# Optimization experiments

Hardware: AMD Instinct MI355X
Metric: run time of the kernel (lower is better)

## Reference

```python
import jax, jax.numpy as jnp
import numpy as np

N_SLOTS = 64
DECAY = 0.999
B, S, H, M = 4, 4096, 2048, 128


def _l2norm(t, eps=1e-12):
    return t / jnp.maximum(jnp.linalg.norm(t, axis=-1, keepdims=True), eps)


def setup_inputs() -> dict:
    key = jax.random.key(0)
    ks = jax.random.split(key, 6)
    return {
        "x": jax.random.normal(ks[0], (B, S, H), dtype=jnp.float32),
        "W_query": jax.random.normal(ks[1], (M, H), dtype=jnp.float32) * 0.02,
        "W_key": jax.random.normal(ks[2], (M, H), dtype=jnp.float32) * 0.02,
        "W_value": jax.random.normal(ks[3], (M, H), dtype=jnp.float32) * 0.02,
        "W_out": jax.random.normal(ks[4], (H, M), dtype=jnp.float32) * 0.02,
        "W_gate_w": jax.random.normal(ks[5], (1, H), dtype=jnp.float32) * 0.02,
        "W_gate_b": jnp.full((1,), -2.0, dtype=jnp.float32),
        "log_beta": jnp.full((1,), np.log(8.0), dtype=jnp.float32),
        "chunk_size": 64,
    }


def reference(x, W_query, W_key, W_value, W_out, W_gate_w, W_gate_b, log_beta, chunk_size):
    b, s, h = x.shape
    m = W_query.shape[0]
    dt = x.dtype

    q = x @ W_query.T                      # (b, s, m)
    k = _l2norm(x @ W_key.T)               # (b, s, m)
    v = _l2norm(x @ W_value.T)             # (b, s, m)
    gate = jax.nn.sigmoid(x @ W_gate_w.T + W_gate_b)  # (b, s, 1)
    beta = jnp.exp(log_beta).reshape(())

    nc = s // chunk_size
    decay_c = jnp.asarray(DECAY, dt) ** chunk_size

    def chunkify(t):
        # (b, s, d) -> (nc, b, chunk, d)
        return jnp.moveaxis(t.reshape(b, nc, chunk_size, -1), 1, 0)

    qc, kc, vc = chunkify(q), chunkify(k), chunkify(v)
    wc = chunkify(gate)[..., 0]            # (nc, b, chunk)

    K0 = jnp.zeros((N_SLOTS, m), dt)
    V0 = jnp.zeros((N_SLOTS, m), dt)
    s0 = jnp.zeros((N_SLOTS,), dt)
    ptr0 = jnp.asarray(0, jnp.int32)

    def step(carry, inp):
        K_mem, V_mem, mem_strength, ptr = carry
        qch, kch, vch, wch = inp           # (b,c,m) x3, (b,c)
        # --- read: softmax retrieval over active slots ---
        slot_mask = (mem_strength > 1e-8).astype(dt)           # (n_slots,)
        scores = jnp.einsum("bcm,nm->bcn", qch, K_mem) * beta
        scores = scores + (1.0 - slot_mask) * -1e9
        attn = jax.nn.softmax(scores, axis=-1)
        r = jnp.einsum("bcn,nm->bcm", attn, V_mem)
        r = jnp.where(mem_strength.sum() < 1e-8, jnp.zeros_like(r), r)
        # --- write: gated aggregation into one slot ---
        w_sum = jnp.maximum(wch.sum(), 1e-8)
        k_agg = _l2norm((kch * wch[..., None]).sum((0, 1)) / w_sum)
        v_agg = _l2norm((vch * wch[..., None]).sum((0, 1)) / w_sum)
        write_str = wch.mean()
        mem_strength = mem_strength * decay_c
        slot = ptr % N_SLOTS
        K_mem = K_mem.at[slot].set(k_agg)
        V_mem = V_mem.at[slot].set(v_agg)
        mem_strength = mem_strength.at[slot].set(write_str)
        return (K_mem, V_mem, mem_strength, ptr + 1), (r, write_str)

    _, (rs, wss) = jax.lax.scan(step, (K0, V0, s0, ptr0), (qc, kc, vc, wc))

    retrieved = jnp.moveaxis(rs, 0, 1).reshape(b, s, m)
    out = retrieved @ W_out.T              # (b, s, h)
    # clamp output norm to 10
    onorm = jnp.maximum(jnp.linalg.norm(out, axis=-1, keepdims=True), 1e-6)
    out = out * jnp.minimum(10.0 / onorm, 1.0)
    mean_ws = jnp.mean(wss)
    return out, mean_ws
```

## Files before the change

### kernel.cpp

```cpp
#include <hip/hip_runtime.h>
#include <math.h>
#include <stdint.h>

#define NTOK 16384
#define SEQ  4096
#define HD   2048
#define MD   128
#define NCH  64
#define CHK  64

typedef __attribute__((ext_vector_type(8))) _Float16 half8;
typedef __attribute__((ext_vector_type(4))) float floatx4;

__device__ __forceinline__ void gload_lds16(const void* g, void* l) {
    __builtin_amdgcn_global_load_lds(
        (const __attribute__((address_space(1))) unsigned int*)(uintptr_t)g,
        (__attribute__((address_space(3))) unsigned int*)(uintptr_t)l,
        16, 0, 0);
}

__global__ __launch_bounds__(256) void convert_w_kernel(
    const float* __restrict__ Wq, const float* __restrict__ Wk,
    const float* __restrict__ Wv, const float* __restrict__ Wo,
    _Float16* __restrict__ Wcath, _Float16* __restrict__ Woh)
{
    int i = blockIdx.x * 256 + threadIdx.x;
    if (i < 384 * HD) {
        int r = i >> 11;
        float val;
        if (r < 128)      val = Wq[i];
        else if (r < 256) val = Wk[i - 128 * HD];
        else              val = Wv[i - 256 * HD];
        Wcath[i] = (_Float16)val;
    } else {
        int j = i - 384 * HD;
        Woh[j] = (_Float16)Wo[j];
    }
}

__global__ __launch_bounds__(128) void gmat_kernel(
    const float* __restrict__ Wo, float* __restrict__ G)
{
    __shared__ float col[HD];
    int a = blockIdx.x;
    int b = threadIdx.x;
    for (int j = b; j < HD; j += 128) col[j] = Wo[(size_t)j * MD + a];
    __syncthreads();
    float s = 0.f;
    for (int j = 0; j < HD; ++j) s = fmaf(col[j], Wo[(size_t)j * MD + b], s);
    G[a * MD + b] = s;
}

__global__ __launch_bounds__(256) void gemm_proj_mfma(
    const float* __restrict__ x, const _Float16* __restrict__ Wcath,
    const float* __restrict__ Wgw, const float* __restrict__ gb,
    float* __restrict__ q, float* __restrict__ k, float* __restrict__ v,
    float* __restrict__ wg)
{
    __shared__ _Float16 As[2048], Bs[4096];
    floatx4 acc[2][4];
    #pragma unroll
    for (int i = 0; i < 2; ++i)
        #pragma unroll
        for (int j = 0; j < 4; ++j) acc[i][j] = (floatx4){0.f, 0.f, 0.f, 0.f};

    const int tid  = threadIdx.x;
    const int wave = tid >> 6, lane = tid & 63;
    const int wm = wave & 1, wn = wave >> 1;
    const int seg_r = lane >> 2;
    const int chunk = lane & 3;
    const int arow  = tid >> 2;
    const int acol  = tid & 3;
    const int row0 = blockIdx.x * 64;
    const int col0 = blockIdx.y * 128;
    const bool do_gate = (blockIdx.y == 0);

    float gacc = 0.f;

    for (int k0 = 0; k0 < HD; k0 += 32) {
        #pragma unroll
        for (int rnd = 0; rnd < 2; ++rnd) {
            int s = wave + 4 * rnd;
            int r = s * 16 + seg_r;
            gload_lds16(Wcath + (size_t)(col0 + r) * HD + k0 + chunk * 8,
                        Bs + s * 512);
        }
        const float* ap = x + (size_t)(row0 + arow) * HD + k0 + acol * 8;
        float4 a0 = *(const float4*)(ap);
        float4 a1 = *(const float4*)(ap + 4);
        if (do_gate) {
            const float* wp = Wgw + k0 + acol * 8;
            float4 w0 = *(const float4*)(wp);
            float4 w1 = *(const float4*)(wp + 4);
            gacc += a0.x * w0.x + a0.y * w0.y + a0.z * w0.z + a0.w * w0.w
                  + a1.x * w1.x + a1.y * w1.y + a1.z * w1.z + a1.w * w1.w;
        }
        half8 h0;
        h0[0] = (_Float16)a0.x; h0[1] = (_Float16)a0.y;
        h0[2] = (_Float16)a0.z; h0[3] = (_Float16)a0.w;
        h0[4] = (_Float16)a1.x; h0[5] = (_Float16)a1.y;
        h0[6] = (_Float16)a1.z; h0[7] = (_Float16)a1.w;
        *(half8*)&As[arow * 32 + acol * 8] = h0;

        __syncthreads();
        half8 af[2], bf[4];
        #pragma unroll
        for (int i = 0; i < 2; ++i)
            af[i] = *(const half8*)&As[(wm * 32 + i * 16 + (lane & 15)) * 32 + (lane >> 4) * 8];
        #pragma unroll
        for (int j = 0; j < 4; ++j)
            bf[j] = *(const half8*)&Bs[(wn * 64 + j * 16 + (lane & 15)) * 32 + (lane >> 4) * 8];
        #pragma unroll
        for (int i = 0; i < 2; ++i)
            #pragma unroll
            for (int j = 0; j < 4; ++j)
                acc[i][j] = __builtin_amdgcn_mfma_f32_16x16x32_f16(
                    af[i], bf[j], acc[i][j], 0, 0, 0);
        __syncthreads();
    }

    if (do_gate) {
        float g4 = gacc + __shfl_xor(gacc, 1);
        g4 += __shfl_xor(g4, 2);
        if (acol == 0) {
            int row = row0 + arow;
            wg[row] = 1.f / (1.f + expf(-(g4 + gb[0])));
        }
    }

    float* dst = (blockIdx.y == 0) ? q : ((blockIdx.y == 1) ? k : v);
    #pragma unroll
    for (int i = 0; i < 2; ++i) {
        int m = row0 + wm * 32 + i * 16 + (lane >> 4) * 4;
        #pragma unroll
        for (int j = 0; j < 4; ++j) {
            int c = wn * 64 + j * 16 + (lane & 15);
            #pragma unroll
            for (int r = 0; r < 4; ++r)
                dst[(size_t)(m + r) * MD + c] = acc[i][j][r];
        }
    }
}

__global__ __launch_bounds__(256) void normsig_kernel(
    float* __restrict__ k, float* __restrict__ v)
{
    int wave = threadIdx.x >> 6, lane = threadIdx.x & 63;
    int row = blockIdx.x * 4 + wave;
    size_t base = (size_t)row * MD + lane * 2;
    float2 k2 = *reinterpret_cast<float2*>(&k[base]);
    float2 v2 = *reinterpret_cast<float2*>(&v[base]);
    float ks = k2.x * k2.x + k2.y * k2.y;
    float vs = v2.x * v2.x + v2.y * v2.y;
    #pragma unroll
    for (int off = 32; off > 0; off >>= 1) {
        ks += __shfl_xor(ks, off);
        vs += __shfl_xor(vs, off);
    }
    float ki = 1.f / fmaxf(sqrtf(ks), 1e-12f);
    float vi = 1.f / fmaxf(sqrtf(vs), 1e-12f);
    k2.x *= ki; k2.y *= ki; v2.x *= vi; v2.y *= vi;
    *reinterpret_cast<float2*>(&k[base]) = k2;
    *reinterpret_cast<float2*>(&v[base]) = v2;
}

__global__ __launch_bounds__(256) void agg_part_kernel(
    const float* __restrict__ kn, const float* __restrict__ vn,
    const float* __restrict__ w,
    float* __restrict__ kpart, float* __restrict__ vpart,
    float* __restrict__ wpart)
{
    int t = blockIdx.x >> 2, b = blockIdx.x & 3;
    int tid = threadIdx.x;
    int d = tid & 127, h = tid >> 7;
    int base_row = b * SEQ + t * CHK;

    float ka = 0.f, va = 0.f;
    for (int c = h * 32; c < h * 32 + 32; ++c) {
        int row = base_row + c;
        float wv = w[row];
        ka = fmaf(wv, kn[(size_t)row * MD + d], ka);
        va = fmaf(wv, vn[(size_t)row * MD + d], va);
    }
    __shared__ float sk[128], sv[128];
    if (h == 1) { sk[d] = ka; sv[d] = va; }
    __syncthreads();
    if (h == 0) {
        kpart[(size_t)blockIdx.x * 128 + d] = ka + sk[d];
        vpart[(size_t)blockIdx.x * 128 + d] = va + sv[d];
    }
    if (tid < 64) {
        float wv = w[base_row + tid];
        #pragma unroll
        for (int off = 32; off > 0; off >>= 1) wv += __shfl_xor(wv, off);
        if (tid == 0) wpart[blockIdx.x] = wv;
    }
}

__global__ __launch_bounds__(128) void agg_combine_kernel(
    const float* __restrict__ kpart, const float* __restrict__ vpart,
    const float* __restrict__ wpart,
    float* __restrict__ kaT, float* __restrict__ vagg, float* __restrict__ wstr)
{
    int t = blockIdx.x;
    int d = threadIdx.x;
    int wave = d >> 6, lane = d & 63;
    float ku = 0.f, vu = 0.f;
    #pragma unroll
    for (int b = 0; b < 4; ++b) {
        ku += kpart[(size_t)(t * 4 + b) * 128 + d];
        vu += vpart[(size_t)(t * 4 + b) * 128 + d];
    }
    float wsum = wpart[t * 4] + wpart[t * 4 + 1] + wpart[t * 4 + 2] + wpart[t * 4 + 3];
    float winv = 1.f / fmaxf(wsum, 1e-8f);
    ku *= winv; vu *= winv;

    __shared__ float red[4];
    float ks = ku * ku, vs = vu * vu;
    #pragma unroll
    for (int off = 32; off > 0; off >>= 1) {
        ks += __shfl_xor(ks, off);
        vs += __shfl_xor(vs, off);
    }
    if (lane == 0) { red[wave] = ks; red[2 + wave] = vs; }
    __syncthreads();
    float kinv = 1.f / fmaxf(sqrtf(red[0] + red[1]), 1e-12f);
    float vinv = 1.f / fmaxf(sqrtf(red[2] + red[3]), 1e-12f);
    kaT[d * NCH + t] = ku * kinv;
    vagg[t * MD + d] = vu * vinv;
    if (d == 0) wstr[t] = wsum * (1.f / 256.f);
}

__global__ __launch_bounds__(64) void meanws_kernel(
    const float* __restrict__ wstr, float* __restrict__ outp)
{
    int lane = threadIdx.x;
    float v = wstr[lane];
    #pragma unroll
    for (int off = 32; off > 0; off >>= 1) v += __shfl_xor(v, off);
    if (lane == 0) outp[0] = v * (1.f / 64.f);
}

__global__ __launch_bounds__(256) void attn_kernel(
    const float* __restrict__ q, const float* __restrict__ kaT,
    const float* __restrict__ vagg, const float* __restrict__ G,
    const float* __restrict__ logbeta, _Float16* __restrict__ rsh16)
{
    __shared__ float qs[4][128];
    __shared__ float attn_s[4][64];
    __shared__ float rsh[4][128];
    int wave = threadIdx.x >> 6, lane = threadIdx.x & 63;
    int row = blockIdx.x * 4 + wave;
    int t = (row & (SEQ - 1)) >> 6;
    float beta = expf(logbeta[0]);

    qs[wave][lane]      = q[(size_t)row * MD + lane];
    qs[wave][lane + 64] = q[(size_t)row * MD + 64 + lane];
    __syncthreads();

    float sc = -INFINITY;
    if (lane < t) {
        sc = 0.f;
        for (int d = 0; d < 128; ++d)
            sc = fmaf(qs[wave][d], kaT[d * NCH + lane], sc);
        sc *= beta;
    }
    float mx = sc;
    #pragma unroll
    for (int off = 32; off > 0; off >>= 1) mx = fmaxf(mx, __shfl_xor(mx, off));
    float e = (lane < t) ? expf(sc - mx) : 0.f;
    float ssum = e;
    #pragma unroll
    for (int off = 32; off > 0; off >>= 1) ssum += __shfl_xor(ssum, off);
    float attn = (t > 0) ? (e / ssum) : 0.f;
    attn_s[wave][lane] = attn;
    __syncthreads();

    float r0 = 0.f, r1 = 0.f;
    for (int n = 0; n < t; ++n) {
        float a = attn_s[wave][n];
        r0 = fmaf(a, vagg[n * MD + lane], r0);
        r1 = fmaf(a, vagg[n * MD + 64 + lane], r1);
    }
    rsh[wave][lane]      = r0;
    rsh[wave][lane + 64] = r1;
    __syncthreads();

    float t0 = 0.f, t1 = 0.f;
    for (int b = 0; b < 128; ++b) {
        float rb = rsh[wave][b];
        t0 = fmaf(G[b * MD + lane], rb, t0);
        t1 = fmaf(G[b * MD + 64 + lane], rb, t1);
    }
    float quad = r0 * t0 + r1 * t1;
    #pragma unroll
    for (int off = 32; off > 0; off >>= 1) quad += __shfl_xor(quad, off);
    float nrm = fmaxf(sqrtf(fmaxf(quad, 0.f)), 1e-6f);
    float scl = fminf(10.f / nrm, 1.f);
    rsh16[(size_t)row * MD + lane]      = (_Float16)(r0 * scl);
    rsh16[(size_t)row * MD + 64 + lane] = (_Float16)(r1 * scl);
}

__global__ __launch_bounds__(256) void gemm_out_mfma(
    const _Float16* __restrict__ rsh16, const _Float16* __restrict__ Woh,
    float* __restrict__ C)
{
    __shared__ _Float16 As[4096], Bs[4096];
    floatx4 acc[4][4];
    #pragma unroll
    for (int i = 0; i < 4; ++i)
        #pragma unroll
        for (int j = 0; j < 4; ++j) acc[i][j] = (floatx4){0.f, 0.f, 0.f, 0.f};

    const int tid  = threadIdx.x;
    const int wave = tid >> 6, lane = tid & 63;
    const int wm = wave & 1, wn = wave >> 1;
    const int seg_r = lane >> 2;
    const int chunk = lane & 3;
    const int row0 = blockIdx.x * 128;
    const int col0 = blockIdx.y * 128;

    for (int k0 = 0; k0 < MD; k0 += 32) {
        #pragma unroll
        for (int rnd = 0; rnd < 2; ++rnd) {
            int s = wave + 4 * rnd;
            int r = s * 16 + seg_r;
            gload_lds16(rsh16 + (size_t)(row0 + r) * MD + k0 + chunk * 8,
                        As + s * 512);
            gload_lds16(Woh + (size_t)(col0 + r) * MD + k0 + chunk * 8,
                        Bs + s * 512);
        }
        __syncthreads();
        half8 af[4], bf[4];
        #pragma unroll
        for (int i = 0; i < 4; ++i) {
            af[i] = *(const half8*)&As[(wm * 64 + i * 16 + (lane & 15)) * 32 + (lane >> 4) * 8];
            bf[i] = *(const half8*)&Bs[(wn * 64 + i * 16 + (lane & 15)) * 32 + (lane >> 4) * 8];
        }
        #pragma unroll
        for (int i = 0; i < 4; ++i)
            #pragma unroll
            for (int j = 0; j < 4; ++j)
                acc[i][j] = __builtin_amdgcn_mfma_f32_16x16x32_f16(
                    af[i], bf[j], acc[i][j], 0, 0, 0);
        __syncthreads();
    }

    #pragma unroll
    for (int i = 0; i < 4; ++i) {
        int m = row0 + wm * 64 + i * 16 + (lane >> 4) * 4;
        #pragma unroll
        for (int j = 0; j < 4; ++j) {
            int c = col0 + wn * 64 + j * 16 + (lane & 15);
            #pragma unroll
            for (int r = 0; r < 4; ++r)
                C[(size_t)(m + r) * HD + c] = acc[i][j][r];
        }
    }
}

extern "C" void kernel_launch(void* const* d_in, const int* in_sizes, int n_in,
                              void* d_out, int out_size, void* d_ws, size_t ws_size,
                              hipStream_t stream)
{
    const float* x   = (const float*)d_in[0];
    const float* Wq  = (const float*)d_in[1];
    const float* Wk  = (const float*)d_in[2];
    const float* Wv  = (const float*)d_in[3];
    const float* Wo  = (const float*)d_in[4];
    const float* Wgw = (const float*)d_in[5];
    const float* Wgb = (const float*)d_in[6];
    const float* lb  = (const float*)d_in[7];
    float* out = (float*)d_out;

    float* q    = (float*)d_ws;
    float* kn   = q + (size_t)NTOK * MD;
    float* vn   = kn + (size_t)NTOK * MD;
    float* wg   = vn + (size_t)NTOK * MD;
    float* kaT  = wg + NTOK;
    float* vagg = kaT + MD * NCH;
    float* wstr = vagg + NCH * MD;
    float* G    = wstr + 64;
    float* kpart = G + MD * MD;
    float* vpart = kpart + 256 * 128;
    float* wpart = vpart + 256 * 128;
    _Float16* Wcath = (_Float16*)(wpart + 256);
    _Float16* Woh   = Wcath + 384 * HD;
    _Float16* rsh16 = Woh + HD * MD;

    convert_w_kernel<<<dim3(4096), dim3(256), 0, stream>>>(Wq, Wk, Wv, Wo, Wcath, Woh);
    gmat_kernel<<<dim3(128), dim3(128), 0, stream>>>(Wo, G);
    gemm_proj_mfma<<<dim3(NTOK / 64, 3), dim3(256), 0, stream>>>(
        x, Wcath, Wgw, Wgb, q, kn, vn, wg);
    normsig_kernel<<<dim3(NTOK / 4), dim3(256), 0, stream>>>(kn, vn);
    agg_part_kernel<<<dim3(256), dim3(256), 0, stream>>>(kn, vn, wg, kpart, vpart, wpart);
    agg_combine_kernel<<<dim3(NCH), dim3(128), 0, stream>>>(kpart, vpart, wpart, kaT, vagg, wstr);
    meanws_kernel<<<dim3(1), dim3(64), 0, stream>>>(wstr, out + (size_t)NTOK * HD);
    attn_kernel<<<dim3(NTOK / 4), dim3(256), 0, stream>>>(q, kaT, vagg, G, lb, rsh16);
    gemm_out_mfma<<<dim3(NTOK / 128, HD / 128), dim3(256), 0, stream>>>(rsh16, Woh, out);
}
```

Baseline: 410.4 us.

## Double-buffer projection GEMM with BK=64 and XOR-swizzled LDS tiles

Rewrites the q/k/v projection GEMM main loop to use double-buffered LDS tiles with a K-step of 64 instead of 32. The next tile's global loads (async LDS loads for weights, register loads for x) are issued before the current tile's MFMAs, and one barrier per iteration replaces two. The LDS layout is XOR-swizzled to avoid bank conflicts, and a launch bound of 3 blocks per CU is added. The cost is more LDS per block and more registers, which could limit occupancy.

```diff
diff --git a/kernel.cpp b/kernel.cpp
--- a/kernel.cpp
+++ b/kernel.cpp
@@ -51,13 +51,14 @@
     G[a * MD + b] = s;
 }
 
-__global__ __launch_bounds__(256) void gemm_proj_mfma(
+__global__ __launch_bounds__(256, 3) void gemm_proj_mfma(
     const float* __restrict__ x, const _Float16* __restrict__ Wcath,
     const float* __restrict__ Wgw, const float* __restrict__ gb,
     float* __restrict__ q, float* __restrict__ k, float* __restrict__ v,
     float* __restrict__ wg)
 {
-    __shared__ _Float16 As[2048], Bs[4096];
+    __shared__ _Float16 As[2][64 * 64];
+    __shared__ _Float16 Bs[2][128 * 64];
     floatx4 acc[2][4];
     #pragma unroll
     for (int i = 0; i < 2; ++i)
@@ -67,64 +68,114 @@
     const int tid  = threadIdx.x;
     const int wave = tid >> 6, lane = tid & 63;
     const int wm = wave & 1, wn = wave >> 1;
-    const int seg_r = lane >> 2;
-    const int chunk = lane & 3;
-    const int arow  = tid >> 2;
-    const int acol  = tid & 3;
     const int row0 = blockIdx.x * 64;
     const int col0 = blockIdx.y * 128;
     const bool do_gate = (blockIdx.y == 0);
 
-    float gacc = 0.f;
-
-    for (int k0 = 0; k0 < HD; k0 += 32) {
-        #pragma unroll
-        for (int rnd = 0; rnd < 2; ++rnd) {
-            int s = wave + 4 * rnd;
-            int r = s * 16 + seg_r;
-            gload_lds16(Wcath + (size_t)(col0 + r) * HD + k0 + chunk * 8,
-                        Bs + s * 512);
-        }
-        const float* ap = x + (size_t)(row0 + arow) * HD + k0 + acol * 8;
-        float4 a0 = *(const float4*)(ap);
-        float4 a1 = *(const float4*)(ap + 4);
-        if (do_gate) {
-            const float* wp = Wgw + k0 + acol * 8;
-            float4 w0 = *(const float4*)(wp);
-            float4 w1 = *(const float4*)(wp + 4);
-            gacc += a0.x * w0.x + a0.y * w0.y + a0.z * w0.z + a0.w * w0.w
-                  + a1.x * w1.x + a1.y * w1.y + a1.z * w1.z + a1.w * w1.w;
-        }
-        half8 h0;
-        h0[0] = (_Float16)a0.x; h0[1] = (_Float16)a0.y;
-        h0[2] = (_Float16)a0.z; h0[3] = (_Float16)a0.w;
-        h0[4] = (_Float16)a1.x; h0[5] = (_Float16)a1.y;
-        h0[6] = (_Float16)a1.z; h0[7] = (_Float16)a1.w;
-        *(half8*)&As[arow * 32 + acol * 8] = h0;
-
+    const int ar0 = tid >> 3;
+    const int ac0 = (tid & 7) ^ (ar0 & 7);
+    const float* xA0 = x + (size_t)(row0 + ar0) * HD + ac0 * 8;
+    const float* xA1 = x + (size_t)(row0 + ar0 + 32) * HD + ac0 * 8;
+    const float* wgp = Wgw + ac0 * 8;
+
+    float gacc0 = 0.f, gacc1 = 0.f;
+    float4 a00, a01, a10, a11, g0, g1;
+
+#define STAGE_B(buf_, k0_) do {                                               \
+        _Pragma("unroll")                                                     \
+        for (int rnd = 0; rnd < 4; ++rnd) {                                   \
+            int sg = rnd * 4 + wave;                                          \
+            int br = sg * 8 + (lane >> 3);                                    \
+            int bc = (lane & 7) ^ (br & 7);                                   \
+            gload_lds16(Wcath + (size_t)(col0 + br) * HD + (k0_) + bc * 8,    \
+                        (char*)Bs[buf_] + sg * 1024);                         \
+        } } while (0)
+
+#define LOAD_A(k0_) do {                                                      \
+        a00 = *(const float4*)(xA0 + (k0_));                                  \
+        a01 = *(const float4*)(xA0 + (k0_) + 4);                              \
+        a10 = *(const float4*)(xA1 + (k0_));                                  \
+        a11 = *(const float4*)(xA1 + (k0_) + 4);                              \
+        if (do_gate) {                                                        \
+            g0 = *(const float4*)(wgp + (k0_));                               \
+            g1 = *(const float4*)(wgp + (k0_) + 4);                           \
+        } } while (0)
+
+#define FINISH_A(buf_) do {                                                   \
+        if (do_gate) {                                                        \
+            gacc0 += a00.x*g0.x + a00.y*g0.y + a00.z*g0.z + a00.w*g0.w        \
+                   + a01.x*g1.x + a01.y*g1.y + a01.z*g1.z + a01.w*g1.w;       \
+            gacc1 += a10.x*g0.x + a10.y*g0.y + a10.z*g0.z + a10.w*g0.w        \
+                   + a11.x*g1.x + a11.y*g1.y + a11.z*g1.z + a11.w*g1.w;       \
+        }                                                                     \
+        half8 h0, h1;                                                         \
+        h0[0] = (_Float16)a00.x; h0[1] = (_Float16)a00.y;                     \
+        h0[2] = (_Float16)a00.z; h0[3] = (_Float16)a00.w;                     \
+        h0[4] = (_Float16)a01.x; h0[5] = (_Float16)a01.y;                     \
+        h0[6] = (_Float16)a01.z; h0[7] = (_Float16)a01.w;                     \
+        h1[0] = (_Float16)a10.x; h1[1] = (_Float16)a10.y;                     \
+        h1[2] = (_Float16)a10.z; h1[3] = (_Float16)a10.w;                     \
+        h1[4] = (_Float16)a11.x; h1[5] = (_Float16)a11.y;                     \
+        h1[6] = (_Float16)a11.z; h1[7] = (_Float16)a11.w;                     \
+        *(half8*)((char*)As[buf_] + tid * 16)        = h0;                    \
+        *(half8*)((char*)As[buf_] + 4096 + tid * 16) = h1;                    \
+    } while (0)
+
+#define COMPUTE(buf_) do {                                                    \
+        half8 af[2][2], bf[4][2];                                             \
+        _Pragma("unroll")                                                     \
+        for (int i = 0; i < 2; ++i) {                                         \
+            int r  = wm * 32 + i * 16 + (lane & 15);                          \
+            int rb = r * 128 + (lane >> 4) * 16;                              \
+            int sw = (r & 7) << 4;                                            \
+            af[i][0] = *(const half8*)((const char*)As[buf_] + ( rb       ^ sw)); \
+            af[i][1] = *(const half8*)((const char*)As[buf_] + ((rb + 64) ^ sw)); \
+        }                                                                     \
+        _Pragma("unroll")                                                     \
+        for (int j = 0; j < 4; ++j) {                                         \
+            int r  = wn * 64 + j * 16 + (lane & 15);                          \
+            int rb = r * 128 + (lane >> 4) * 16;                              \
+            int sw = (r & 7) << 4;                                            \
+            bf[j][0] = *(const half8*)((const char*)Bs[buf_] + ( rb       ^ sw)); \
+            bf[j][1] = *(const half8*)((const char*)Bs[buf_] + ((rb + 64) ^ sw)); \
+        }                                                                     \
+        _Pragma("unroll")                                                     \
+        for (int ks = 0; ks < 2; ++ks)                                        \
+            _Pragma("unroll")                                                 \
+            for (int i = 0; i < 2; ++i)                                       \
+                _Pragma("unroll")                                             \
+                for (int j = 0; j < 4; ++j)                                   \
+                    acc[i][j] = __builtin_amdgcn_mfma_f32_16x16x32_f16(       \
+                        af[i][ks], bf[j][ks], acc[i][j], 0, 0, 0);            \
+    } while (0)
+
+    STAGE_B(0, 0);
+    LOAD_A(0);
+    FINISH_A(0);
+    __syncthreads();
+
+    int cur = 0;
+    for (int t = 0; t < HD / 64; ++t) {
+        if (t < HD / 64 - 1) {
+            STAGE_B(cur ^ 1, (t + 1) * 64);
+            LOAD_A((t + 1) * 64);
+        }
+        COMPUTE(cur);
+        if (t < HD / 64 - 1) FINISH_A(cur ^ 1);
         __syncthreads();
-        half8 af[2], bf[4];
-        #pragma unroll
-        for (int i = 0; i < 2; ++i)
-            af[i] = *(const half8*)&As[(wm * 32 + i * 16 + (lane & 15)) * 32 + (lane >> 4) * 8];
-        #pragma unroll
-        for (int j = 0; j < 4; ++j)
-            bf[j] = *(const half8*)&Bs[(wn * 64 + j * 16 + (lane & 15)) * 32 + (lane >> 4) * 8];
-        #pragma unroll
-        for (int i = 0; i < 2; ++i)
-            #pragma unroll
-            for (int j = 0; j < 4; ++j)
-                acc[i][j] = __builtin_amdgcn_mfma_f32_16x16x32_f16(
-                    af[i], bf[j], acc[i][j], 0, 0, 0);
-        __syncthreads();
+        cur ^= 1;
     }
 
     if (do_gate) {
-        float g4 = gacc + __shfl_xor(gacc, 1);
-        g4 += __shfl_xor(g4, 2);
-        if (acol == 0) {
-            int row = row0 + arow;
-            wg[row] = 1.f / (1.f + expf(-(g4 + gb[0])));
+        gacc0 += __shfl_xor(gacc0, 1);
+        gacc0 += __shfl_xor(gacc0, 2);
+        gacc0 += __shfl_xor(gacc0, 4);
+        gacc1 += __shfl_xor(gacc1, 1);
+        gacc1 += __shfl_xor(gacc1, 2);
+        gacc1 += __shfl_xor(gacc1, 4);
+        if ((tid & 7) == 0) {
+            wg[row0 + ar0]      = 1.f / (1.f + expf(-(gacc0 + gb[0])));
+            wg[row0 + ar0 + 32] = 1.f / (1.f + expf(-(gacc1 + gb[0])));
         }
     }
 
@@ -140,6 +191,10 @@
                 dst[(size_t)(m + r) * MD + c] = acc[i][j][r];
         }
     }
+#undef STAGE_B
+#undef LOAD_A
+#undef FINISH_A
+#undef COMPUTE
 }
 
 __global__ __launch_bounds__(256) void normsig_kernel(
```

Result: faster. 394.6 us (-3.9%).
